# Optimization experiments

Hardware: AMD Instinct MI355X
Metric: run time of the kernel (lower is better)

The kernel has to match this reference:

```python
import jax, jax.numpy as jnp
import numpy as np

DIM = 256
HEADS = 8
WH, WW = 7, 7
N = WH * WW
B_ = 2048


def _relative_position_index(wh, ww):
    coords = np.stack(np.meshgrid(np.arange(wh), np.arange(ww), indexing='ij'))  # (2,wh,ww)
    cf = coords.reshape(2, -1)  # (2, N)
    rel = cf[:, :, None] - cf[:, None, :]  # (2, N, N)
    rel = rel.transpose(1, 2, 0).astype(np.int32)
    rel[:, :, 0] += wh - 1
    rel[:, :, 1] += ww - 1
    rel[:, :, 0] *= 2 * ww - 1
    return rel.sum(-1)  # (N, N) int32


def setup_inputs() -> dict:
    key = jax.random.key(0)
    ks = jax.random.split(key, 7)
    return {
        'x1': jax.random.normal(ks[0], (B_, N, DIM), jnp.float32),
        'x2': jax.random.normal(ks[1], (B_, N, DIM), jnp.float32),
        'qkv_w': jax.random.normal(ks[2], (3 * DIM, DIM), jnp.float32) * 0.02,
        'qkv_b': jax.random.normal(ks[3], (3 * DIM,), jnp.float32) * 0.02,
        'proj_w': jax.random.normal(ks[4], (DIM, DIM), jnp.float32) * 0.02,
        'proj_b': jax.random.normal(ks[5], (DIM,), jnp.float32) * 0.02,
        'rpb_table': jax.random.normal(ks[6], ((2 * WH - 1) * (2 * WW - 1), HEADS), jnp.float32) * 0.02,
        'rel_index': jnp.asarray(_relative_position_index(WH, WW)),
    }


def reference(x1, x2, qkv_w, qkv_b, proj_w, proj_b, rpb_table, rel_index):
    B, n, C = x1.shape
    H = HEADS
    d = C // H
    scale = d ** (-0.5)

    def qkv(x):
        y = x @ qkv_w.T + qkv_b  # (B, N, 3C)
        y = y.reshape(B, n, 3, H, d).transpose(2, 0, 3, 1, 4)  # (3, B, H, N, d)
        return y[0], y[1], y[2]

    q1, _, _ = qkv(x1)
    _, k2, v2 = qkv(x2)

    attn = jnp.einsum('bhnd,bhmd->bhnm', q1 * scale, k2)  # (B, H, N, N)
    bias = rpb_table[rel_index]  # (N, N, H)
    attn = attn + bias.transpose(2, 0, 1)[None]  # broadcast over batch
    attn = jax.nn.softmax(attn, axis=-1)

    out = jnp.einsum('bhnm,bhmd->bhnd', attn, v2)  # (B, H, N, d)
    out = out.transpose(0, 2, 1, 3).reshape(B, n, C)
    return out @ proj_w.T + proj_b
```

## Files before the change

kernel.cpp:

```cpp
#include <hip/hip_runtime.h>
#include <hip/hip_bf16.h>

#define NTOK 49
#define NP 64
#define CDIM 256
#define NH 8
#define SCALE 0.17677669529663687f

#define SX_BYTES 32768
#define SV_BYTES 32768
#define SP_BYTES 16384

using f32x4  = __attribute__((ext_vector_type(4))) float;
using bf16x8 = __attribute__((ext_vector_type(8))) short;

__device__ __forceinline__ unsigned f2bf_u(float f) {
  union { float f; unsigned u; } c; c.f = f;
  return (c.u + 0x7fffu + ((c.u >> 16) & 1u)) >> 16;
}
__device__ __forceinline__ unsigned pk2(float a, float b) {
  return f2bf_u(a) | (f2bf_u(b) << 16);
}

__device__ __forceinline__ int sx_b(int row, int col) {
  return (row * 512 + col * 2) ^ ((row & 7) << 4);
}
__device__ __forceinline__ int sv_b(int feat, int tok) {
  return (feat * 128 + tok * 2) ^ ((feat & 7) << 4);
}
__device__ __forceinline__ int sp_b(int w, int row, int key) {
  return w * 2048 + ((row * 128 + key * 2) ^ ((row & 7) << 4));
}
__device__ __forceinline__ int so_b(int row, int col) {
  return (row * 512 + col * 4) ^ ((row & 7) << 4);
}

__global__ void prep_kernel(const float* __restrict__ qkv_w, const float* __restrict__ qkv_b,
                            const float* __restrict__ proj_w,
                            const float* __restrict__ rpb, const int* __restrict__ rel,
                            short* __restrict__ wqkv, short* __restrict__ wp,
                            float* __restrict__ bias_s, float* __restrict__ bias_att) {
  int i = blockIdx.x * 256 + threadIdx.x;
  if (i < 768 * 256) {
    int j = i >> 8;
    float v = qkv_w[i] * (j < 256 ? SCALE : 1.0f);
    wqkv[i] = (short)f2bf_u(v);
    return;
  }
  i -= 768 * 256;
  if (i < 256 * 256) { wp[i] = (short)f2bf_u(proj_w[i]); return; }
  i -= 256 * 256;
  if (i < 768) { bias_s[i] = qkv_b[i] * (i < 256 ? SCALE : 1.0f); return; }
  i -= 768;
  if (i < NH * NP * NP) {
    int h = i >> 12, rem = i & 4095, r = rem >> 6, c = rem & 63;
    float v;
    if (c >= NTOK)      v = -1e30f;
    else if (r >= NTOK) v = 0.0f;
    else                v = rpb[rel[r * NTOK + c] * NH + h];
    bias_att[i] = v;
  }
}

__device__ __forceinline__ void gemm32(const char* sxc, const short* __restrict__ wg,
                                       const float* __restrict__ bias,
                                       f32x4 acc[4][2], int w, int lr, int lg) {
  const short* wr0 = wg + (w * 32 + lr) * CDIM + lg * 8;
  const short* wr1 = wg + (w * 32 + 16 + lr) * CDIM + lg * 8;
  const float bv0 = bias[w * 32 + lr];
  const float bv1 = bias[w * 32 + 16 + lr];
  #pragma unroll
  for (int rt = 0; rt < 4; ++rt) {
    #pragma unroll
    for (int r = 0; r < 4; ++r) { acc[rt][0][r] = bv0; acc[rt][1][r] = bv1; }
  }
  #pragma unroll
  for (int k = 0; k < 8; ++k) {
    const bf16x8 b0 = *(const bf16x8*)(wr0 + k * 32);
    const bf16x8 b1 = *(const bf16x8*)(wr1 + k * 32);
    #pragma unroll
    for (int rt = 0; rt < 4; ++rt) {
      const bf16x8 af = *(const bf16x8*)(sxc + sx_b(rt * 16 + lr, k * 32 + lg * 8));
      acc[rt][0] = __builtin_amdgcn_mfma_f32_16x16x32_bf16(af, b0, acc[rt][0], 0, 0, 0);
      acc[rt][1] = __builtin_amdgcn_mfma_f32_16x16x32_bf16(af, b1, acc[rt][1], 0, 0, 0);
    }
  }
}

__global__ __launch_bounds__(512) __attribute__((amdgpu_waves_per_eu(4, 4)))
void fused_attn(const float* __restrict__ x1, const float* __restrict__ x2,
                const short* __restrict__ wqkv, const float* __restrict__ bias_s,
                const short* __restrict__ wp, const float* __restrict__ proj_b,
                const float* __restrict__ bias_att, float* __restrict__ out) {
  extern __shared__ char ldsc[];
  char* sxc = ldsc;
  char* svc = ldsc + SX_BYTES;
  char* spc = ldsc + SX_BYTES + SV_BYTES;

  const int tid = threadIdx.x;
  const int w = tid >> 6, lane = tid & 63;
  const int lr = lane & 15, lg = lane >> 4;
  const int b = blockIdx.x;
  const int r0 = (w >> 1) * 16;
  const int hb = (w & 1) * 4;

  {
    const float* xg = x1 + (size_t)b * NTOK * CDIM;
    #pragma unroll
    for (int it = 0; it < 8; ++it) {
      const int i = tid + it * 512;
      const int row = i >> 6, c4 = i & 63;
      uint2 pkv = make_uint2(0u, 0u);
      if (row < NTOK) {
        const float4 v = *(const float4*)(xg + row * CDIM + c4 * 4);
        pkv.x = pk2(v.x, v.y); pkv.y = pk2(v.z, v.w);
      }
      *(uint2*)(sxc + sx_b(row, c4 * 4)) = pkv;
    }
  }
  __syncthreads();

  f32x4 acc[4][2];

  gemm32(sxc, wqkv, bias_s, acc, w, lr, lg);
  __syncthreads();
  #pragma unroll
  for (int rt = 0; rt < 4; ++rt)
    #pragma unroll
    for (int ct = 0; ct < 2; ++ct)
      #pragma unroll
      for (int r = 0; r < 4; ++r)
        *(short*)(sxc + sx_b(rt * 16 + lg * 4 + r, w * 32 + ct * 16 + lr)) =
            (short)f2bf_u(acc[rt][ct][r]);
  __syncthreads();

  bf16x8 qa[4];
  #pragma unroll
  for (int hh = 0; hh < 4; ++hh)
    qa[hh] = *(const bf16x8*)(sxc + sx_b(r0 + lr, (hb + hh) * 32 + lg * 8));
  __syncthreads();

  {
    const float* xg = x2 + (size_t)b * NTOK * CDIM;
    #pragma unroll
    for (int it = 0; it < 8; ++it) {
      const int i = tid + it * 512;
      const int row = i >> 6, c4 = i & 63;
      uint2 pkv = make_uint2(0u, 0u);
      if (row < NTOK) {
        const float4 v = *(const float4*)(xg + row * CDIM + c4 * 4);
        pkv.x = pk2(v.x, v.y); pkv.y = pk2(v.z, v.w);
      }
      *(uint2*)(sxc + sx_b(row, c4 * 4)) = pkv;
    }
  }
  __syncthreads();

  gemm32(sxc, wqkv + 512 * CDIM, bias_s + 512, acc, w, lr, lg);
  #pragma unroll
  for (int rt = 0; rt < 4; ++rt)
    #pragma unroll
    for (int ct = 0; ct < 2; ++ct) {
      uint2 pkv = make_uint2(pk2(acc[rt][ct][0], acc[rt][ct][1]),
                             pk2(acc[rt][ct][2], acc[rt][ct][3]));
      *(uint2*)(svc + sv_b(w * 32 + ct * 16 + lr, rt * 16 + lg * 4)) = pkv;
    }

  gemm32(sxc, wqkv + 256 * CDIM, bias_s + 256, acc, w, lr, lg);
  __syncthreads();
  #pragma unroll
  for (int rt = 0; rt < 4; ++rt)
    #pragma unroll
    for (int ct = 0; ct < 2; ++ct)
      #pragma unroll
      for (int r = 0; r < 4; ++r)
        *(short*)(sxc + sx_b(rt * 16 + lg * 4 + r, w * 32 + ct * 16 + lr)) =
            (short)f2bf_u(acc[rt][ct][r]);
  __syncthreads();

  f32x4 oacc[4][2];
  #pragma unroll
  for (int hh = 0; hh < 4; ++hh)
    #pragma unroll
    for (int jt = 0; jt < 2; ++jt) {
      oacc[hh][jt][0] = 0; oacc[hh][jt][1] = 0; oacc[hh][jt][2] = 0; oacc[hh][jt][3] = 0;
    }

  #pragma unroll
  for (int hh = 0; hh < 4; ++hh) {
    const int h = hb + hh;
    const float* bh = bias_att + h * NP * NP + r0 * NP;
    f32x4 s[4];
    #pragma unroll
    for (int ct = 0; ct < 4; ++ct) {
      f32x4 sb;
      #pragma unroll
      for (int r = 0; r < 4; ++r) sb[r] = bh[(lg * 4 + r) * NP + ct * 16 + lr];
      const bf16x8 kb = *(const bf16x8*)(sxc + sx_b(ct * 16 + lr, h * 32 + lg * 8));
      s[ct] = __builtin_amdgcn_mfma_f32_16x16x32_bf16(qa[hh], kb, sb, 0, 0, 0);
    }
    float mx[4], si[4];
    #pragma unroll
    for (int r = 0; r < 4; ++r) {
      float m = fmaxf(fmaxf(s[0][r], s[1][r]), fmaxf(s[2][r], s[3][r]));
      m = fmaxf(m, __shfl_xor(m, 1, 64));
      m = fmaxf(m, __shfl_xor(m, 2, 64));
      m = fmaxf(m, __shfl_xor(m, 4, 64));
      m = fmaxf(m, __shfl_xor(m, 8, 64));
      mx[r] = m;
    }
    #pragma unroll
    for (int ct = 0; ct < 4; ++ct)
      #pragma unroll
      for (int r = 0; r < 4; ++r)
        s[ct][r] = __expf(s[ct][r] - mx[r]);
    #pragma unroll
    for (int r = 0; r < 4; ++r) {
      float t = s[0][r] + s[1][r] + s[2][r] + s[3][r];
      t += __shfl_xor(t, 1, 64);
      t += __shfl_xor(t, 2, 64);
      t += __shfl_xor(t, 4, 64);
      t += __shfl_xor(t, 8, 64);
      si[r] = __builtin_amdgcn_rcpf(t);
    }
    #pragma unroll
    for (int ct = 0; ct < 4; ++ct)
      #pragma unroll
      for (int r = 0; r < 4; ++r)
        *(short*)(spc + sp_b(w, lg * 4 + r, ct * 16 + lr)) =
            (short)f2bf_u(s[ct][r] * si[r]);
    #pragma unroll
    for (int kk = 0; kk < 2; ++kk) {
      const bf16x8 pa = *(const bf16x8*)(spc + sp_b(w, lr, kk * 32 + lg * 8));
      #pragma unroll
      for (int jt = 0; jt < 2; ++jt) {
        const bf16x8 vb = *(const bf16x8*)(svc + sv_b(h * 32 + jt * 16 + lr, kk * 32 + lg * 8));
        oacc[hh][jt] = __builtin_amdgcn_mfma_f32_16x16x32_bf16(pa, vb, oacc[hh][jt], 0, 0, 0);
      }
    }
  }

  __syncthreads();
  #pragma unroll
  for (int hh = 0; hh < 4; ++hh)
    #pragma unroll
    for (int jt = 0; jt < 2; ++jt)
      #pragma unroll
      for (int r = 0; r < 4; ++r)
        *(short*)(sxc + sx_b(r0 + lg * 4 + r, (hb + hh) * 32 + jt * 16 + lr)) =
            (short)f2bf_u(oacc[hh][jt][r]);
  __syncthreads();

  gemm32(sxc, wp, proj_b, acc, w, lr, lg);

  float* og = out + (size_t)b * NTOK * CDIM;
  #pragma unroll
  for (int half = 0; half < 2; ++half) {
    if ((w >> 2) == half) {
      const int wc = (w & 3) * 32;
      #pragma unroll
      for (int rt = 0; rt < 4; ++rt)
        #pragma unroll
        for (int ct = 0; ct < 2; ++ct)
          #pragma unroll
          for (int r = 0; r < 4; ++r)
            *(float*)(svc + so_b(rt * 16 + lg * 4 + r, wc + ct * 16 + lr)) = acc[rt][ct][r];
    }
    __syncthreads();
    for (int i = tid; i < NTOK * 32; i += 512) {
      const int row = i >> 5, c4 = i & 31;
      const float4 v = *(const float4*)(svc + so_b(row, c4 * 4));
      *(float4*)(og + row * CDIM + half * 128 + c4 * 4) = v;
    }
    __syncthreads();
  }
}

extern "C" void kernel_launch(void* const* d_in, const int* in_sizes, int n_in,
                              void* d_out, int out_size, void* d_ws, size_t ws_size,
                              hipStream_t stream) {
  const float* x1     = (const float*)d_in[0];
  const float* x2     = (const float*)d_in[1];
  const float* qkv_w  = (const float*)d_in[2];
  const float* qkv_b  = (const float*)d_in[3];
  const float* proj_w = (const float*)d_in[4];
  const float* proj_b = (const float*)d_in[5];
  const float* rpb    = (const float*)d_in[6];
  const int*   rel    = (const int*)d_in[7];

  char* ws = (char*)d_ws;
  short* wqkv     = (short*)ws;
  short* wp       = (short*)(ws + 768 * 256 * 2);
  float* bias_s   = (float*)(ws + 768 * 256 * 2 + 256 * 256 * 2);
  float* bias_att = (float*)(ws + 768 * 256 * 2 + 256 * 256 * 2 + 768 * 4);

  const int prep_total = 768 * 256 + 256 * 256 + 768 + NH * NP * NP;
  prep_kernel<<<(prep_total + 255) / 256, 256, 0, stream>>>(
      qkv_w, qkv_b, proj_w, rpb, rel, wqkv, wp, bias_s, bias_att);

  const int Bn = in_sizes[0] / (NTOK * CDIM);
  const size_t shmem = SX_BYTES + SV_BYTES + SP_BYTES;
  (void)hipFuncSetAttribute((const void*)fused_attn,
                            hipFuncAttributeMaxDynamicSharedMemorySize, (int)shmem);
  fused_attn<<<Bn, 512, shmem, stream>>>(x1, x2, wqkv, bias_s, wp, proj_b, bias_att,
                                         (float*)d_out);
}
```

Before: 307.2 us.

## Split fused attention into QKV projection and attention+projection kernels via workspace

Adds a qkv_kernel that computes Q1, K2 and V2 in bf16 per window and writes them to a global workspace image. A separate 256-thread attnproj_kernel then reads them back to do softmax attention and the output projection. The intent is to shrink per-block LDS and register pressure so occupancy rises, replacing the single large fused kernel. This adds a second launch and a global-memory round trip of roughly 96 KB per window. The old fused kernel is kept as a fallback when the workspace is too small.

Measured after the change: 290.8 us. 1.06x faster.

```diff
diff --git a/kernel.cpp b/kernel.cpp
--- a/kernel.cpp
+++ b/kernel.cpp
@@ -87,6 +87,227 @@
   }
 }
 
+template <int NT>
+__device__ __forceinline__ void stage_x(char* sxc, const float* __restrict__ xg, int tid) {
+  #pragma unroll
+  for (int it = 0; it < 4096 / NT; ++it) {
+    const int i = tid + it * NT;
+    const int row = i >> 6, c4 = i & 63;
+    uint2 pkv = make_uint2(0u, 0u);
+    if (row < NTOK) {
+      const float4 v = *(const float4*)(xg + row * CDIM + c4 * 4);
+      pkv.x = pk2(v.x, v.y); pkv.y = pk2(v.z, v.w);
+    }
+    *(uint2*)(sxc + sx_b(row, c4 * 4)) = pkv;
+  }
+}
+
+#define IMG_STRIDE 98304
+
+__global__ __launch_bounds__(512) __attribute__((amdgpu_waves_per_eu(4, 4)))
+void qkv_kernel(const float* __restrict__ x1, const float* __restrict__ x2,
+                const short* __restrict__ wqkv, const float* __restrict__ bias_s,
+                char* __restrict__ img) {
+  extern __shared__ char ldsc[];
+  char* sxc = ldsc;
+  char* stc = ldsc + 32768;
+
+  const int tid = threadIdx.x;
+  const int w = tid >> 6, lane = tid & 63;
+  const int lr = lane & 15, lg = lane >> 4;
+  const int b = blockIdx.x;
+  char* wsb = img + (size_t)b * IMG_STRIDE;
+
+  f32x4 acc[4][2];
+
+  stage_x<512>(sxc, x1 + (size_t)b * NTOK * CDIM, tid);
+  __syncthreads();
+
+  gemm32(sxc, wqkv, bias_s, acc, w, lr, lg);
+  #pragma unroll
+  for (int rt = 0; rt < 4; ++rt)
+    #pragma unroll
+    for (int ct = 0; ct < 2; ++ct)
+      #pragma unroll
+      for (int r = 0; r < 4; ++r)
+        *(short*)(stc + sx_b(rt * 16 + lg * 4 + r, w * 32 + ct * 16 + lr)) =
+            (short)f2bf_u(acc[rt][ct][r]);
+  __syncthreads();
+
+  #pragma unroll
+  for (int it = 0; it < 4; ++it) {
+    const int i = tid + it * 512;
+    *(float4*)(wsb + i * 16) = *(const float4*)(stc + i * 16);
+  }
+  stage_x<512>(sxc, x2 + (size_t)b * NTOK * CDIM, tid);
+  __syncthreads();
+
+  gemm32(sxc, wqkv + 512 * CDIM, bias_s + 512, acc, w, lr, lg);
+  #pragma unroll
+  for (int rt = 0; rt < 4; ++rt)
+    #pragma unroll
+    for (int ct = 0; ct < 2; ++ct) {
+      uint2 pkv = make_uint2(pk2(acc[rt][ct][0], acc[rt][ct][1]),
+                             pk2(acc[rt][ct][2], acc[rt][ct][3]));
+      *(uint2*)(stc + sv_b(w * 32 + ct * 16 + lr, rt * 16 + lg * 4)) = pkv;
+    }
+  __syncthreads();
+
+  #pragma unroll
+  for (int it = 0; it < 4; ++it) {
+    const int i = tid + it * 512;
+    *(float4*)(wsb + 65536 + i * 16) = *(const float4*)(stc + i * 16);
+  }
+  gemm32(sxc, wqkv + 256 * CDIM, bias_s + 256, acc, w, lr, lg);
+  __syncthreads();
+
+  #pragma unroll
+  for (int rt = 0; rt < 4; ++rt)
+    #pragma unroll
+    for (int ct = 0; ct < 2; ++ct)
+      #pragma unroll
+      for (int r = 0; r < 4; ++r)
+        *(short*)(stc + sx_b(rt * 16 + lg * 4 + r, w * 32 + ct * 16 + lr)) =
+            (short)f2bf_u(acc[rt][ct][r]);
+  __syncthreads();
+
+  #pragma unroll
+  for (int it = 0; it < 4; ++it) {
+    const int i = tid + it * 512;
+    *(float4*)(wsb + 32768 + i * 16) = *(const float4*)(stc + i * 16);
+  }
+}
+
+__global__ __launch_bounds__(256) __attribute__((amdgpu_waves_per_eu(4, 4)))
+void attnproj_kernel(const char* __restrict__ img, const short* __restrict__ wp,
+                     const float* __restrict__ proj_b, const float* __restrict__ bias_att,
+                     float* __restrict__ out) {
+  extern __shared__ char ldsc[];
+  char* soc = ldsc;
+  char* spc = ldsc + 32768;
+
+  const int tid = threadIdx.x;
+  const int w = tid >> 6, lane = tid & 63;
+  const int lr = lane & 15, lg = lane >> 4;
+  const int b = blockIdx.x;
+  const char* qimg = img + (size_t)b * IMG_STRIDE;
+  const char* kimg = qimg + 32768;
+  const char* vimg = qimg + 65536;
+
+  #pragma unroll
+  for (int hh = 0; hh < 2; ++hh) {
+    const int h = w * 2 + hh;
+    bf16x8 kb[4];
+    #pragma unroll
+    for (int ct = 0; ct < 4; ++ct)
+      kb[ct] = *(const bf16x8*)(kimg + sx_b(ct * 16 + lr, h * 32 + lg * 8));
+    bf16x8 vb[2][2];
+    #pragma unroll
+    for (int kk = 0; kk < 2; ++kk)
+      #pragma unroll
+      for (int jt = 0; jt < 2; ++jt)
+        vb[kk][jt] = *(const bf16x8*)(vimg + sv_b(h * 32 + jt * 16 + lr, kk * 32 + lg * 8));
+    const float* bh = bias_att + h * NP * NP;
+
+    #pragma unroll
+    for (int qt = 0; qt < 4; ++qt) {
+      const bf16x8 qa = *(const bf16x8*)(qimg + sx_b(qt * 16 + lr, h * 32 + lg * 8));
+      f32x4 s[4];
+      #pragma unroll
+      for (int ct = 0; ct < 4; ++ct) {
+        f32x4 sb;
+        #pragma unroll
+        for (int r = 0; r < 4; ++r) sb[r] = bh[(qt * 16 + lg * 4 + r) * NP + ct * 16 + lr];
+        s[ct] = __builtin_amdgcn_mfma_f32_16x16x32_bf16(qa, kb[ct], sb, 0, 0, 0);
+      }
+      float mx[4], si[4];
+      #pragma unroll
+      for (int r = 0; r < 4; ++r) {
+        float m = fmaxf(fmaxf(s[0][r], s[1][r]), fmaxf(s[2][r], s[3][r]));
+        m = fmaxf(m, __shfl_xor(m, 1, 64));
+        m = fmaxf(m, __shfl_xor(m, 2, 64));
+        m = fmaxf(m, __shfl_xor(m, 4, 64));
+        m = fmaxf(m, __shfl_xor(m, 8, 64));
+        mx[r] = m;
+      }
+      #pragma unroll
+      for (int ct = 0; ct < 4; ++ct)
+        #pragma unroll
+        for (int r = 0; r < 4; ++r)
+          s[ct][r] = __expf(s[ct][r] - mx[r]);
+      #pragma unroll
+      for (int r = 0; r < 4; ++r) {
+        float t = s[0][r] + s[1][r] + s[2][r] + s[3][r];
+        t += __shfl_xor(t, 1, 64);
+        t += __shfl_xor(t, 2, 64);
+        t += __shfl_xor(t, 4, 64);
+        t += __shfl_xor(t, 8, 64);
+        si[r] = __builtin_amdgcn_rcpf(t);
+      }
+      #pragma unroll
+      for (int ct = 0; ct < 4; ++ct)
+        #pragma unroll
+        for (int r = 0; r < 4; ++r)
+          *(short*)(spc + sp_b(w, lg * 4 + r, ct * 16 + lr)) =
+              (short)f2bf_u(s[ct][r] * si[r]);
+      f32x4 oq[2];
+      #pragma unroll
+      for (int jt = 0; jt < 2; ++jt) { oq[jt][0] = 0; oq[jt][1] = 0; oq[jt][2] = 0; oq[jt][3] = 0; }
+      #pragma unroll
+      for (int kk = 0; kk < 2; ++kk) {
+        const bf16x8 pa = *(const bf16x8*)(spc + sp_b(w, lr, kk * 32 + lg * 8));
+        #pragma unroll
+        for (int jt = 0; jt < 2; ++jt)
+          oq[jt] = __builtin_amdgcn_mfma_f32_16x16x32_bf16(pa, vb[kk][jt], oq[jt], 0, 0, 0);
+      }
+      #pragma unroll
+      for (int jt = 0; jt < 2; ++jt)
+        #pragma unroll
+        for (int r = 0; r < 4; ++r)
+          *(short*)(soc + sx_b(qt * 16 + lg * 4 + r, h * 32 + jt * 16 + lr)) =
+              (short)f2bf_u(oq[jt][r]);
+    }
+  }
+  __syncthreads();
+
+  float* og = out + (size_t)b * NTOK * CDIM;
+  #pragma unroll
+  for (int p = 0; p < 2; ++p) {
+    const int c0 = w * 64 + p * 32;
+    const short* wr0 = wp + (c0 + lr) * CDIM + lg * 8;
+    const short* wr1 = wp + (c0 + 16 + lr) * CDIM + lg * 8;
+    const float bv0 = proj_b[c0 + lr];
+    const float bv1 = proj_b[c0 + 16 + lr];
+    f32x4 acc[4][2];
+    #pragma unroll
+    for (int rt = 0; rt < 4; ++rt)
+      #pragma unroll
+      for (int r = 0; r < 4; ++r) { acc[rt][0][r] = bv0; acc[rt][1][r] = bv1; }
+    #pragma unroll
+    for (int k = 0; k < 8; ++k) {
+      const bf16x8 b0 = *(const bf16x8*)(wr0 + k * 32);
+      const bf16x8 b1 = *(const bf16x8*)(wr1 + k * 32);
+      #pragma unroll
+      for (int rt = 0; rt < 4; ++rt) {
+        const bf16x8 af = *(const bf16x8*)(soc + sx_b(rt * 16 + lr, k * 32 + lg * 8));
+        acc[rt][0] = __builtin_amdgcn_mfma_f32_16x16x32_bf16(af, b0, acc[rt][0], 0, 0, 0);
+        acc[rt][1] = __builtin_amdgcn_mfma_f32_16x16x32_bf16(af, b1, acc[rt][1], 0, 0, 0);
+      }
+    }
+    #pragma unroll
+    for (int rt = 0; rt < 4; ++rt)
+      #pragma unroll
+      for (int r = 0; r < 4; ++r) {
+        const int row = rt * 16 + lg * 4 + r;
+        if (row < NTOK) {
+          #pragma unroll
+          for (int ct = 0; ct < 2; ++ct)
+            og[row * CDIM + c0 + ct * 16 + lr] = acc[rt][ct][r];
+        }
+      }
+  }
+}
+
 __global__ __launch_bounds__(512) __attribute__((amdgpu_waves_per_eu(4, 4)))
 void fused_attn(const float* __restrict__ x1, const float* __restrict__ x2,
                 const short* __restrict__ wqkv, const float* __restrict__ bias_s,
@@ -104,24 +325,10 @@
   const int r0 = (w >> 1) * 16;
   const int hb = (w & 1) * 4;
 
-  {
-    const float* xg = x1 + (size_t)b * NTOK * CDIM;
-    #pragma unroll
-    for (int it = 0; it < 8; ++it) {
-      const int i = tid + it * 512;
-      const int row = i >> 6, c4 = i & 63;
-      uint2 pkv = make_uint2(0u, 0u);
-      if (row < NTOK) {
-        const float4 v = *(const float4*)(xg + row * CDIM + c4 * 4);
-        pkv.x = pk2(v.x, v.y); pkv.y = pk2(v.z, v.w);
-      }
-      *(uint2*)(sxc + sx_b(row, c4 * 4)) = pkv;
-    }
-  }
+  stage_x<512>(sxc, x1 + (size_t)b * NTOK * CDIM, tid);
   __syncthreads();
 
   f32x4 acc[4][2];
-
   gemm32(sxc, wqkv, bias_s, acc, w, lr, lg);
   __syncthreads();
   #pragma unroll
@@ -140,20 +347,7 @@
     qa[hh] = *(const bf16x8*)(sxc + sx_b(r0 + lr, (hb + hh) * 32 + lg * 8));
   __syncthreads();
 
-  {
-    const float* xg = x2 + (size_t)b * NTOK * CDIM;
-    #pragma unroll
-    for (int it = 0; it < 8; ++it) {
-      const int i = tid + it * 512;
-      const int row = i >> 6, c4 = i & 63;
-      uint2 pkv = make_uint2(0u, 0u);
-      if (row < NTOK) {
-        const float4 v = *(const float4*)(xg + row * CDIM + c4 * 4);
-        pkv.x = pk2(v.x, v.y); pkv.y = pk2(v.z, v.w);
-      }
-      *(uint2*)(sxc + sx_b(row, c4 * 4)) = pkv;
-    }
-  }
+  stage_x<512>(sxc, x2 + (size_t)b * NTOK * CDIM, tid);
   __syncthreads();
 
   gemm32(sxc, wqkv + 512 * CDIM, bias_s + 512, acc, w, lr, lg);
@@ -290,18 +484,30 @@
 
   char* ws = (char*)d_ws;
   short* wqkv     = (short*)ws;
-  short* wp       = (short*)(ws + 768 * 256 * 2);
-  float* bias_s   = (float*)(ws + 768 * 256 * 2 + 256 * 256 * 2);
-  float* bias_att = (float*)(ws + 768 * 256 * 2 + 256 * 256 * 2 + 768 * 4);
+  short* wp       = (short*)(ws + 393216);
+  float* bias_s   = (float*)(ws + 524288);
+  float* bias_att = (float*)(ws + 527360);
+  char*  img      = ws + 658432;
 
   const int prep_total = 768 * 256 + 256 * 256 + 768 + NH * NP * NP;
   prep_kernel<<<(prep_total + 255) / 256, 256, 0, stream>>>(
       qkv_w, qkv_b, proj_w, rpb, rel, wqkv, wp, bias_s, bias_att);
 
   const int Bn = in_sizes[0] / (NTOK * CDIM);
-  const size_t shmem = SX_BYTES + SV_BYTES + SP_BYTES;
-  (void)hipFuncSetAttribute((const void*)fused_attn,
-                            hipFuncAttributeMaxDynamicSharedMemorySize, (int)shmem);
-  fused_attn<<<Bn, 512, shmem, stream>>>(x1, x2, wqkv, bias_s, wp, proj_b, bias_att,
-                                         (float*)d_out);
-}
+  const size_t need = 658432 + (size_t)Bn * IMG_STRIDE;
+
+  if (ws_size >= need) {
+    (void)hipFuncSetAttribute((const void*)qkv_kernel,
+                              hipFuncAttributeMaxDynamicSharedMemorySize, 65536);
+    (void)hipFuncSetAttribute((const void*)attnproj_kernel,
+                              hipFuncAttributeMaxDynamicSharedMemorySize, 40960);
+    qkv_kernel<<<Bn, 512, 65536, stream>>>(x1, x2, wqkv, bias_s, img);
+    attnproj_kernel<<<Bn, 256, 40960, stream>>>(img, wp, proj_b, bias_att, (float*)d_out);
+  } else {
+    const size_t shmem = SX_BYTES + SV_BYTES + SP_BYTES;
+    (void)hipFuncSetAttribute((const void*)fused_attn,
+                              hipFuncAttributeMaxDynamicSharedMemorySize, (int)shmem);
+    fused_attn<<<Bn, 512, shmem, stream>>>(x1, x2, wqkv, bias_s, wp, proj_b, bias_att,
+                                           (float*)d_out);
+  }
+}
```

## Assign one head per wave so QKV and attention stay in per-wave LDS tiles

Applied to the files above, without the earlier changes.

Each wave now computes the Q, K and V columns of its own head and keeps them in a private 4 KB LDS tile. That removes several block-wide barriers and shrinks LDS from 80 KB to 64 KB, with launch bounds asking for 2 blocks per CU. The attention bias table is stored transposed so bias loads become float4, K and V fragments are held in registers, and the output is written straight from the accumulators instead of being staged through LDS. In exchange, the global stores become scalar and strided, and register pressure rises from the extra held fragments.

Measured after the change: 320.6 us. 4.4% more time.

```diff
diff --git a/kernel.cpp b/kernel.cpp
--- a/kernel.cpp
+++ b/kernel.cpp
@@ -7,10 +7,6 @@
 #define NH 8
 #define SCALE 0.17677669529663687f
 
-#define SX_BYTES 32768
-#define SV_BYTES 32768
-#define SP_BYTES 16384
-
 using f32x4  = __attribute__((ext_vector_type(4))) float;
 using bf16x8 = __attribute__((ext_vector_type(8))) short;
 
@@ -25,14 +21,14 @@
 __device__ __forceinline__ int sx_b(int row, int col) {
   return (row * 512 + col * 2) ^ ((row & 7) << 4);
 }
-__device__ __forceinline__ int sv_b(int feat, int tok) {
+__device__ __forceinline__ int rm_b(int row, int col) {
+  return (row * 64 + col * 2) ^ ((row & 7) << 4);
+}
+__device__ __forceinline__ int vt_b(int feat, int tok) {
   return (feat * 128 + tok * 2) ^ ((feat & 7) << 4);
 }
-__device__ __forceinline__ int sp_b(int w, int row, int key) {
-  return w * 2048 + ((row * 128 + key * 2) ^ ((row & 7) << 4));
-}
-__device__ __forceinline__ int so_b(int row, int col) {
-  return (row * 512 + col * 4) ^ ((row & 7) << 4);
+__device__ __forceinline__ int p_b(int q, int tok) {
+  return (q * 128 + tok * 2) ^ ((q & 7) << 4);
 }
 
 __global__ void prep_kernel(const float* __restrict__ qkv_w, const float* __restrict__ qkv_b,
@@ -53,7 +49,7 @@
   if (i < 768) { bias_s[i] = qkv_b[i] * (i < 256 ? SCALE : 1.0f); return; }
   i -= 768;
   if (i < NH * NP * NP) {
-    int h = i >> 12, rem = i & 4095, r = rem >> 6, c = rem & 63;
+    int h = i >> 12, rem = i & 4095, c = rem >> 6, r = rem & 63;
     float v;
     if (c >= NTOK)      v = -1e30f;
     else if (r >= NTOK) v = 0.0f;
@@ -62,13 +58,13 @@
   }
 }
 
-__device__ __forceinline__ void gemm32(const char* sxc, const short* __restrict__ wg,
-                                       const float* __restrict__ bias,
-                                       f32x4 acc[4][2], int w, int lr, int lg) {
-  const short* wr0 = wg + (w * 32 + lr) * CDIM + lg * 8;
-  const short* wr1 = wg + (w * 32 + 16 + lr) * CDIM + lg * 8;
-  const float bv0 = bias[w * 32 + lr];
-  const float bv1 = bias[w * 32 + 16 + lr];
+__device__ __forceinline__ void gemm32c(const char* sxc, const short* __restrict__ wg,
+                                        const float* __restrict__ bias,
+                                        f32x4 acc[4][2], int col0, int lr, int lg) {
+  const short* wr0 = wg + (col0 + lr) * CDIM + lg * 8;
+  const short* wr1 = wg + (col0 + 16 + lr) * CDIM + lg * 8;
+  const float bv0 = bias[col0 + lr];
+  const float bv1 = bias[col0 + 16 + lr];
   #pragma unroll
   for (int rt = 0; rt < 4; ++rt) {
     #pragma unroll
@@ -87,117 +83,102 @@
   }
 }
 
-__global__ __launch_bounds__(512) __attribute__((amdgpu_waves_per_eu(4, 4)))
-void fused_attn(const float* __restrict__ x1, const float* __restrict__ x2,
-                const short* __restrict__ wqkv, const float* __restrict__ bias_s,
-                const short* __restrict__ wp, const float* __restrict__ proj_b,
-                const float* __restrict__ bias_att, float* __restrict__ out) {
-  extern __shared__ char ldsc[];
-  char* sxc = ldsc;
-  char* svc = ldsc + SX_BYTES;
-  char* spc = ldsc + SX_BYTES + SV_BYTES;
+__device__ __forceinline__ void stage_x(char* sxc, const float* __restrict__ xg, int tid) {
+  #pragma unroll
+  for (int it = 0; it < 8; ++it) {
+    const int i = tid + it * 512;
+    const int row = i >> 6, c4 = i & 63;
+    uint2 pkv = make_uint2(0u, 0u);
+    if (row < NTOK) {
+      const float4 v = *(const float4*)(xg + row * CDIM + c4 * 4);
+      pkv.x = pk2(v.x, v.y); pkv.y = pk2(v.z, v.w);
+    }
+    *(uint2*)(sxc + sx_b(row, c4 * 4)) = pkv;
+  }
+}
+
+__device__ __forceinline__ void acc_to_rm(char* pt, const f32x4 acc[4][2], int lr, int lg) {
+  #pragma unroll
+  for (int rt = 0; rt < 4; ++rt)
+    #pragma unroll
+    for (int ct = 0; ct < 2; ++ct)
+      #pragma unroll
+      for (int r = 0; r < 4; ++r)
+        *(short*)(pt + rm_b(rt * 16 + lg * 4 + r, ct * 16 + lr)) =
+            (short)f2bf_u(acc[rt][ct][r]);
+}
+
+__global__ __launch_bounds__(512, 2)
+void fused2(const float* __restrict__ x1, const float* __restrict__ x2,
+            const short* __restrict__ wqkv, const float* __restrict__ bias_s,
+            const short* __restrict__ wp, const float* __restrict__ proj_b,
+            const float* __restrict__ bias_att, float* __restrict__ out) {
+  extern __shared__ char lds[];
+  char* sxc = lds;
+  char* pat = lds + 32768;
 
   const int tid = threadIdx.x;
   const int w = tid >> 6, lane = tid & 63;
   const int lr = lane & 15, lg = lane >> 4;
   const int b = blockIdx.x;
-  const int r0 = (w >> 1) * 16;
-  const int hb = (w & 1) * 4;
-
-  {
-    const float* xg = x1 + (size_t)b * NTOK * CDIM;
-    #pragma unroll
-    for (int it = 0; it < 8; ++it) {
-      const int i = tid + it * 512;
-      const int row = i >> 6, c4 = i & 63;
-      uint2 pkv = make_uint2(0u, 0u);
-      if (row < NTOK) {
-        const float4 v = *(const float4*)(xg + row * CDIM + c4 * 4);
-        pkv.x = pk2(v.x, v.y); pkv.y = pk2(v.z, v.w);
-      }
-      *(uint2*)(sxc + sx_b(row, c4 * 4)) = pkv;
-    }
-  }
+  char* pt = pat + w * 4096;
+
+  stage_x(sxc, x1 + (size_t)b * NTOK * CDIM, tid);
   __syncthreads();
 
   f32x4 acc[4][2];
 
-  gemm32(sxc, wqkv, bias_s, acc, w, lr, lg);
-  __syncthreads();
-  #pragma unroll
-  for (int rt = 0; rt < 4; ++rt)
-    #pragma unroll
-    for (int ct = 0; ct < 2; ++ct)
-      #pragma unroll
-      for (int r = 0; r < 4; ++r)
-        *(short*)(sxc + sx_b(rt * 16 + lg * 4 + r, w * 32 + ct * 16 + lr)) =
-            (short)f2bf_u(acc[rt][ct][r]);
-  __syncthreads();
-
+  gemm32c(sxc, wqkv, bias_s, acc, w * 32, lr, lg);
+  acc_to_rm(pt, acc, lr, lg);
+  __syncthreads();
   bf16x8 qa[4];
   #pragma unroll
-  for (int hh = 0; hh < 4; ++hh)
-    qa[hh] = *(const bf16x8*)(sxc + sx_b(r0 + lr, (hb + hh) * 32 + lg * 8));
-  __syncthreads();
-
-  {
-    const float* xg = x2 + (size_t)b * NTOK * CDIM;
-    #pragma unroll
-    for (int it = 0; it < 8; ++it) {
-      const int i = tid + it * 512;
-      const int row = i >> 6, c4 = i & 63;
-      uint2 pkv = make_uint2(0u, 0u);
-      if (row < NTOK) {
-        const float4 v = *(const float4*)(xg + row * CDIM + c4 * 4);
-        pkv.x = pk2(v.x, v.y); pkv.y = pk2(v.z, v.w);
-      }
-      *(uint2*)(sxc + sx_b(row, c4 * 4)) = pkv;
-    }
-  }
-  __syncthreads();
-
-  gemm32(sxc, wqkv + 512 * CDIM, bias_s + 512, acc, w, lr, lg);
+  for (int qt = 0; qt < 4; ++qt)
+    qa[qt] = *(const bf16x8*)(pt + rm_b(qt * 16 + lr, lg * 8));
+
+  stage_x(sxc, x2 + (size_t)b * NTOK * CDIM, tid);
+  __syncthreads();
+
+  gemm32c(sxc, wqkv + 512 * CDIM, bias_s + 512, acc, w * 32, lr, lg);
   #pragma unroll
   for (int rt = 0; rt < 4; ++rt)
     #pragma unroll
     for (int ct = 0; ct < 2; ++ct) {
       uint2 pkv = make_uint2(pk2(acc[rt][ct][0], acc[rt][ct][1]),
                              pk2(acc[rt][ct][2], acc[rt][ct][3]));
-      *(uint2*)(svc + sv_b(w * 32 + ct * 16 + lr, rt * 16 + lg * 4)) = pkv;
-    }
-
-  gemm32(sxc, wqkv + 256 * CDIM, bias_s + 256, acc, w, lr, lg);
-  __syncthreads();
-  #pragma unroll
-  for (int rt = 0; rt < 4; ++rt)
-    #pragma unroll
-    for (int ct = 0; ct < 2; ++ct)
-      #pragma unroll
-      for (int r = 0; r < 4; ++r)
-        *(short*)(sxc + sx_b(rt * 16 + lg * 4 + r, w * 32 + ct * 16 + lr)) =
-            (short)f2bf_u(acc[rt][ct][r]);
-  __syncthreads();
-
+      *(uint2*)(pt + vt_b(ct * 16 + lr, rt * 16 + lg * 4)) = pkv;
+    }
+  bf16x8 vb[2][2];
+  #pragma unroll
+  for (int kk = 0; kk < 2; ++kk)
+    #pragma unroll
+    for (int jt = 0; jt < 2; ++jt)
+      vb[kk][jt] = *(const bf16x8*)(pt + vt_b(jt * 16 + lr, kk * 32 + lg * 8));
+
+  gemm32c(sxc, wqkv + 256 * CDIM, bias_s + 256, acc, w * 32, lr, lg);
+  acc_to_rm(pt, acc, lr, lg);
+  bf16x8 kb[4];
+  #pragma unroll
+  for (int ct = 0; ct < 4; ++ct)
+    kb[ct] = *(const bf16x8*)(pt + rm_b(ct * 16 + lr, lg * 8));
+
+  const float* bht = bias_att + w * NP * NP;
   f32x4 oacc[4][2];
   #pragma unroll
-  for (int hh = 0; hh < 4; ++hh)
+  for (int qt = 0; qt < 4; ++qt)
     #pragma unroll
     for (int jt = 0; jt < 2; ++jt) {
-      oacc[hh][jt][0] = 0; oacc[hh][jt][1] = 0; oacc[hh][jt][2] = 0; oacc[hh][jt][3] = 0;
-    }
-
-  #pragma unroll
-  for (int hh = 0; hh < 4; ++hh) {
-    const int h = hb + hh;
-    const float* bh = bias_att + h * NP * NP + r0 * NP;
+      oacc[qt][jt][0] = 0; oacc[qt][jt][1] = 0; oacc[qt][jt][2] = 0; oacc[qt][jt][3] = 0;
+    }
+
+  #pragma unroll 1
+  for (int qt = 0; qt < 4; ++qt) {
     f32x4 s[4];
     #pragma unroll
     for (int ct = 0; ct < 4; ++ct) {
-      f32x4 sb;
-      #pragma unroll
-      for (int r = 0; r < 4; ++r) sb[r] = bh[(lg * 4 + r) * NP + ct * 16 + lr];
-      const bf16x8 kb = *(const bf16x8*)(sxc + sx_b(ct * 16 + lr, h * 32 + lg * 8));
-      s[ct] = __builtin_amdgcn_mfma_f32_16x16x32_bf16(qa[hh], kb, sb, 0, 0, 0);
+      const float4 sbv = *(const float4*)(bht + (ct * 16 + lr) * NP + qt * 16 + lg * 4);
+      f32x4 sb; sb[0] = sbv.x; sb[1] = sbv.y; sb[2] = sbv.z; sb[3] = sbv.w;
+      s[ct] = __builtin_amdgcn_mfma_f32_16x16x32_bf16(qa[qt], kb[ct], sb, 0, 0, 0);
     }
     float mx[4], si[4];
     #pragma unroll
@@ -227,52 +208,60 @@
     for (int ct = 0; ct < 4; ++ct)
       #pragma unroll
       for (int r = 0; r < 4; ++r)
-        *(short*)(spc + sp_b(w, lg * 4 + r, ct * 16 + lr)) =
+        *(short*)(pt + p_b(lg * 4 + r, ct * 16 + lr)) =
             (short)f2bf_u(s[ct][r] * si[r]);
     #pragma unroll
     for (int kk = 0; kk < 2; ++kk) {
-      const bf16x8 pa = *(const bf16x8*)(spc + sp_b(w, lr, kk * 32 + lg * 8));
-      #pragma unroll
-      for (int jt = 0; jt < 2; ++jt) {
-        const bf16x8 vb = *(const bf16x8*)(svc + sv_b(h * 32 + jt * 16 + lr, kk * 32 + lg * 8));
-        oacc[hh][jt] = __builtin_amdgcn_mfma_f32_16x16x32_bf16(pa, vb, oacc[hh][jt], 0, 0, 0);
+      const bf16x8 pa = *(const bf16x8*)(pt + p_b(lr, kk * 32 + lg * 8));
+      #pragma unroll
+      for (int jt = 0; jt < 2; ++jt)
+        oacc[qt][jt] = __builtin_amdgcn_mfma_f32_16x16x32_bf16(pa, vb[kk][jt], oacc[qt][jt], 0, 0, 0);
+    }
+  }
+
+  #pragma unroll
+  for (int qt = 0; qt < 4; ++qt)
+    #pragma unroll
+    for (int jt = 0; jt < 2; ++jt)
+      #pragma unroll
+      for (int r = 0; r < 4; ++r)
+        *(short*)(pt + rm_b(qt * 16 + lg * 4 + r, jt * 16 + lr)) =
+            (short)f2bf_u(oacc[qt][jt][r]);
+  __syncthreads();
+
+  {
+    const short* wr0 = wp + (w * 32 + lr) * CDIM + lg * 8;
+    const short* wr1 = wp + (w * 32 + 16 + lr) * CDIM + lg * 8;
+    const float bv0 = proj_b[w * 32 + lr];
+    const float bv1 = proj_b[w * 32 + 16 + lr];
+    #pragma unroll
+    for (int rt = 0; rt < 4; ++rt) {
+      #pragma unroll
+      for (int r = 0; r < 4; ++r) { acc[rt][0][r] = bv0; acc[rt][1][r] = bv1; }
+    }
+    #pragma unroll
+    for (int k = 0; k < 8; ++k) {
+      const bf16x8 b0 = *(const bf16x8*)(wr0 + k * 32);
+      const bf16x8 b1 = *(const bf16x8*)(wr1 + k * 32);
+      #pragma unroll
+      for (int rt = 0; rt < 4; ++rt) {
+        const bf16x8 af = *(const bf16x8*)(pat + k * 4096 + rm_b(rt * 16 + lr, lg * 8));
+        acc[rt][0] = __builtin_amdgcn_mfma_f32_16x16x32_bf16(af, b0, acc[rt][0], 0, 0, 0);
+        acc[rt][1] = __builtin_amdgcn_mfma_f32_16x16x32_bf16(af, b1, acc[rt][1], 0, 0, 0);
       }
     }
-  }
-
-  __syncthreads();
-  #pragma unroll
-  for (int hh = 0; hh < 4; ++hh)
-    #pragma unroll
-    for (int jt = 0; jt < 2; ++jt)
-      #pragma unroll
-      for (int r = 0; r < 4; ++r)
-        *(short*)(sxc + sx_b(r0 + lg * 4 + r, (hb + hh) * 32 + jt * 16 + lr)) =
-            (short)f2bf_u(oacc[hh][jt][r]);
-  __syncthreads();
-
-  gemm32(sxc, wp, proj_b, acc, w, lr, lg);
-
-  float* og = out + (size_t)b * NTOK * CDIM;
-  #pragma unroll
-  for (int half = 0; half < 2; ++half) {
-    if ((w >> 2) == half) {
-      const int wc = (w & 3) * 32;
-      #pragma unroll
-      for (int rt = 0; rt < 4; ++rt)
-        #pragma unroll
-        for (int ct = 0; ct < 2; ++ct)
+    float* og = out + (size_t)b * NTOK * CDIM;
+    #pragma unroll
+    for (int rt = 0; rt < 4; ++rt)
+      #pragma unroll
+      for (int r = 0; r < 4; ++r) {
+        const int row = rt * 16 + lg * 4 + r;
+        if (row < NTOK) {
           #pragma unroll
-          for (int r = 0; r < 4; ++r)
-            *(float*)(svc + so_b(rt * 16 + lg * 4 + r, wc + ct * 16 + lr)) = acc[rt][ct][r];
-    }
-    __syncthreads();
-    for (int i = tid; i < NTOK * 32; i += 512) {
-      const int row = i >> 5, c4 = i & 31;
-      const float4 v = *(const float4*)(svc + so_b(row, c4 * 4));
-      *(float4*)(og + row * CDIM + half * 128 + c4 * 4) = v;
-    }
-    __syncthreads();
+          for (int ct = 0; ct < 2; ++ct)
+            og[row * CDIM + w * 32 + ct * 16 + lr] = acc[rt][ct][r];
+        }
+      }
   }
 }
 
@@ -290,18 +279,18 @@
 
   char* ws = (char*)d_ws;
   short* wqkv     = (short*)ws;
-  short* wp       = (short*)(ws + 768 * 256 * 2);
-  float* bias_s   = (float*)(ws + 768 * 256 * 2 + 256 * 256 * 2);
-  float* bias_att = (float*)(ws + 768 * 256 * 2 + 256 * 256 * 2 + 768 * 4);
+  short* wp       = (short*)(ws + 393216);
+  float* bias_s   = (float*)(ws + 524288);
+  float* bias_att = (float*)(ws + 527360);
 
   const int prep_total = 768 * 256 + 256 * 256 + 768 + NH * NP * NP;
   prep_kernel<<<(prep_total + 255) / 256, 256, 0, stream>>>(
       qkv_w, qkv_b, proj_w, rpb, rel, wqkv, wp, bias_s, bias_att);
 
   const int Bn = in_sizes[0] / (NTOK * CDIM);
-  const size_t shmem = SX_BYTES + SV_BYTES + SP_BYTES;
-  (void)hipFuncSetAttribute((const void*)fused_attn,
+  const size_t shmem = 32768 + 8 * 4096;
+  (void)hipFuncSetAttribute((const void*)fused2,
                             hipFuncAttributeMaxDynamicSharedMemorySize, (int)shmem);
-  fused_attn<<<Bn, 512, shmem, stream>>>(x1, x2, wqkv, bias_s, wp, proj_b, bias_att,
-                                         (float*)d_out);
-}
+  fused2<<<Bn, 512, shmem, stream>>>(x1, x2, wqkv, bias_s, wp, proj_b, bias_att,
+                                     (float*)d_out);
+}
```
